# Kernel optimization log

Measured on AMD Instinct MI355X. Metric: run time of the kernel, lower is better.

The kernel has to match this reference:

```python
import jax, jax.numpy as jnp
import numpy as np

H = 256        # hidden_channels
G = 13         # num_input_geofeature
E = 100000     # number of 2nd-order triplets
N = 50000      # num_nodes
DEPTH = 3      # finaldepth
EPS = 1e-5     # BatchNorm eps


def setup_inputs() -> dict:
    key = jax.random.key(0)
    ks = jax.random.split(key, 10)
    d_in = 3 * H + G  # 781
    return {
        "node_feature": jax.random.normal(ks[0], (N, H), jnp.float32),
        "geo_encoding": jax.random.normal(ks[1], (E, G), jnp.float32),
        "edge_index_2rd": jax.random.randint(ks[2], (3, E), 0, N),
        "edx_ij": jax.random.randint(ks[3], (E,), 0, 2 * E),
        "edx_jk": jax.random.randint(ks[4], (E,), 0, 2 * E),
        "att": jax.random.uniform(ks[5], (4,), jnp.float32),
        # 4 branches: layer0 (d_in->H) + DEPTH layers (H->H), xavier-ish init, zero bias
        "W0": jax.random.normal(ks[6], (4, d_in, H), jnp.float32) * (1.0 / np.sqrt(d_in)),
        "b0": jnp.zeros((4, H), jnp.float32),
        "Wh": jax.random.normal(ks[7], (4, DEPTH, H, H), jnp.float32) * (1.0 / np.sqrt(H)),
        "bh": jnp.zeros((4, DEPTH, H), jnp.float32),
        # BatchNorm (eval mode): affine params + running stats, one per layer per branch
        "gamma": jnp.ones((4, DEPTH + 1, H), jnp.float32),
        "beta": jnp.zeros((4, DEPTH + 1, H), jnp.float32),
        "run_mean": jnp.zeros((4, DEPTH + 1, H), jnp.float32),
        "run_var": jnp.ones((4, DEPTH + 1, H), jnp.float32),
        "num_edge_inside": E,
        "num_nodes": N,
    }


def _bn(h, g, b, m, v):
    return (h - m) * jax.lax.rsqrt(v + EPS) * g + b


def reference(node_feature, geo_encoding, edge_index_2rd, edx_ij, edx_jk, att,
              W0, b0, Wh, bh, gamma, beta, run_mean, run_var,
              num_edge_inside, num_nodes):
    i, j, k = edge_index_2rd[0], edge_index_2rd[1], edge_index_2rd[2]
    # gather node triplets + geo features -> [E, 3H+G]
    x = jnp.concatenate(
        [node_feature[i], node_feature[j], node_feature[k], geo_encoding], axis=-1)

    m_ij = edx_ij < num_edge_inside
    m_jk = edx_jk < num_edge_inside
    # 4 mutually-exclusive, exhaustive routing masks: [4, E]
    masks = jnp.stack([m_ij & m_jk, m_ij & ~m_jk, ~m_ij & m_jk, ~m_ij & ~m_jk])

    x_output = jnp.zeros((x.shape[0], H), x.dtype)
    for br in range(4):  # fixed small branch count
        h = jax.nn.relu(_bn(x @ W0[br] + b0[br],
                            gamma[br, 0], beta[br, 0], run_mean[br, 0], run_var[br, 0]))
        for l in range(DEPTH):
            h = jax.nn.relu(_bn(h @ Wh[br, l] + bh[br, l],
                                gamma[br, l + 1], beta[br, l + 1],
                                run_mean[br, l + 1], run_var[br, l + 1]))
        h = jax.nn.leaky_relu(h) * att[br]
        x_output = x_output + jnp.where(masks[br][:, None], h, jnp.zeros((), h.dtype))
    # scatter_add over target node index i -> [num_nodes, H]
    return jax.ops.segment_sum(x_output, i, num_segments=num_nodes)
```

## Files before the change

kernel.cpp:

```cpp
#include <hip/hip_runtime.h>
#include <hip/hip_bf16.h>
#include <stdint.h>

#define HCH 256
#define GEO 13
#define DEPTH 3
#define EPSBN 1e-5f
#define MFMA __builtin_amdgcn_mfma_f32_16x16x32_bf16

typedef __attribute__((ext_vector_type(8))) short short8;
typedef __attribute__((ext_vector_type(4))) float floatx4;

__device__ __forceinline__ short f2bs(float f) {
    unsigned u = __float_as_uint(f);
    unsigned r = (u + 0x7fffu + ((u >> 16) & 1u)) >> 16;
    return (short)r;
}

__global__ void k_prep(const float* __restrict__ W0, const float* __restrict__ Wh,
                       const float* __restrict__ b0, const float* __restrict__ bh,
                       const float* __restrict__ gm, const float* __restrict__ bt,
                       const float* __restrict__ mn, const float* __restrict__ vr,
                       const float* __restrict__ att,
                       const float* __restrict__ node, const float* __restrict__ geo,
                       const int* __restrict__ edx_ij, const int* __restrict__ edx_jk,
                       const int* __restrict__ nei_p,
                       short* __restrict__ W0t, short* __restrict__ Wht,
                       float* __restrict__ sc, float* __restrict__ of,
                       short* __restrict__ node_bf, short* __restrict__ geo_bf,
                       int* __restrict__ lists, int* __restrict__ cnt,
                       float4* __restrict__ outz, int n4out,
                       int E, int d_in_dim, int nb_node, int nb_geo, int nb_out) {
    const int B_W0 = 100, B_WH = 96, B_SC = 16;
    __shared__ short s[32][256];
    int b = blockIdx.x, t = threadIdx.x;
    if (b < B_W0) {
        int c = b % 25, br = b / 25;
        #pragma unroll
        for (int kk = 0; kk < 32; ++kk) {
            int kidx = c * 32 + kk;
            float v = (kidx < d_in_dim) ? W0[((size_t)br * d_in_dim + kidx) * HCH + t] : 0.f;
            s[kk][t] = f2bs(v);
        }
        __syncthreads();
        size_t obase = ((size_t)(b) * 256 + t) * 32;
        #pragma unroll
        for (int g = 0; g < 4; ++g) {
            short8 v;
            #pragma unroll
            for (int j = 0; j < 8; ++j) v[j] = s[g * 8 + j][t];
            *reinterpret_cast<short8*>(W0t + obase + g * 8) = v;
        }
    } else if (b < B_W0 + B_WH) {
        int idx = b - B_W0;
        int c = idx & 7; idx >>= 3;
        int l = idx % 3, br = idx / 3;
        #pragma unroll
        for (int kk = 0; kk < 32; ++kk) {
            float v = Wh[((size_t)(br * DEPTH + l) * HCH + (c * 32 + kk)) * HCH + t];
            s[kk][t] = f2bs(v);
        }
        __syncthreads();
        size_t obase = ((size_t)(b - B_W0) * 256 + t) * 32;
        #pragma unroll
        for (int g = 0; g < 4; ++g) {
            short8 v;
            #pragma unroll
            for (int j = 0; j < 8; ++j) v[j] = s[g * 8 + j][t];
            *reinterpret_cast<short8*>(Wht + obase + g * 8) = v;
        }
    } else if (b < B_W0 + B_WH + B_SC) {
        int idx = (b - B_W0 - B_WH) * 256 + t;
        int col = idx & 255, l = (idx >> 8) & 3, br = idx >> 10;
        int gi = (br * (DEPTH + 1) + l) * HCH + col;
        float sA = gm[gi] * rsqrtf(vr[gi] + EPSBN);
        float bias = (l == 0) ? b0[br * HCH + col] : bh[(br * DEPTH + (l - 1)) * HCH + col];
        float ofv = (bias - mn[gi]) * sA + bt[gi];
        if (l == 3) { float av = att[br]; sA *= av; ofv *= av; }
        sc[idx] = sA;
        of[idx] = ofv;
    } else if (b < B_W0 + B_WH + B_SC + nb_node) {
        size_t i = ((size_t)(b - B_W0 - B_WH - B_SC) * 256 + t) * 8;
        const float4* src = reinterpret_cast<const float4*>(node + i);
        float4 v0 = src[0], v1 = src[1];
        short8 pk;
        pk[0] = f2bs(v0.x); pk[1] = f2bs(v0.y); pk[2] = f2bs(v0.z); pk[3] = f2bs(v0.w);
        pk[4] = f2bs(v1.x); pk[5] = f2bs(v1.y); pk[6] = f2bs(v1.z); pk[7] = f2bs(v1.w);
        *reinterpret_cast<short8*>(node_bf + i) = pk;
    } else if (b < B_W0 + B_WH + B_SC + nb_node + nb_geo) {
        int i = (b - B_W0 - B_WH - B_SC - nb_node) * 256 + t;
        int e = i >> 2, cc = i & 3;
        if (e < E) {
            short8 pk;
            #pragma unroll
            for (int j = 0; j < 8; ++j) {
                int col = cc * 8 + j;
                pk[j] = (col < GEO) ? f2bs(geo[(size_t)e * GEO + col]) : (short)0;
            }
            *reinterpret_cast<short8*>(geo_bf + (size_t)e * 32 + cc * 8) = pk;
        }
    } else if (b < B_W0 + B_WH + B_SC + nb_node + nb_geo + nb_out) {
        int i = (b - (B_W0 + B_WH + B_SC + nb_node + nb_geo)) * 256 + t;
        if (i < n4out) outz[i] = make_float4(0.f, 0.f, 0.f, 0.f);
    } else {
        int e = (b - (B_W0 + B_WH + B_SC + nb_node + nb_geo + nb_out)) * 256 + t;
        int NEI = nei_p[0];
        int lane = t & 63;
        int br = -1;
        if (e < E)
            br = ((edx_ij[e] < NEI) ? 0 : 2) + ((edx_jk[e] < NEI) ? 0 : 1);
        unsigned long long lt = (lane == 63) ? 0x7fffffffffffffffull
                                             : ((1ull << lane) - 1ull);
        #pragma unroll
        for (int bb = 0; bb < 4; ++bb) {
            unsigned long long mk = __ballot(br == bb);
            if (mk) {
                int leader = __ffsll((long long)mk) - 1;
                int base = 0;
                if (lane == leader) base = atomicAdd(&cnt[bb], (int)__popcll(mk));
                base = __shfl(base, leader);
                if (br == bb) {
                    int pos = base + (int)__popcll(mk & lt);
                    lists[(size_t)bb * E + pos] = e;
                }
            }
        }
    }
}

__global__ __launch_bounds__(512)
void k_main(const short* __restrict__ node_bf, const short* __restrict__ geo_bf,
            const int* __restrict__ eidx,
            const short* __restrict__ W0t, const short* __restrict__ Wht,
            const float* __restrict__ sc, const float* __restrict__ of,
            const int* __restrict__ lists, const int* __restrict__ cnt,
            float* __restrict__ out, int E) {
    __shared__ __align__(16) short A[64][264];
    __shared__ __align__(16) short Ageo[64][40];
    __shared__ int s_idx[3][64];
    __shared__ int s_e[64];

    int nwg = gridDim.x;
    int q = nwg >> 3, r = nwg & 7;
    int xcd = blockIdx.x & 7, jj = blockIdx.x >> 3;
    int b = ((xcd < r) ? xcd * (q + 1) : r * (q + 1) + (xcd - r) * q) + jj;

    int c0 = cnt[0], c1 = cnt[1], c2 = cnt[2], c3 = cnt[3];
    int t0 = (c0 + 63) >> 6, t1 = (c1 + 63) >> 6, t2 = (c2 + 63) >> 6, t3 = (c3 + 63) >> 6;
    int br, tile, count;
    if (b < t0)                     { br = 0; tile = b;                count = c0; }
    else if (b < t0 + t1)           { br = 1; tile = b - t0;           count = c1; }
    else if (b < t0 + t1 + t2)      { br = 2; tile = b - t0 - t1;      count = c2; }
    else if (b < t0 + t1 + t2 + t3) { br = 3; tile = b - t0 - t1 - t2; count = c3; }
    else return;
    int m = count - tile * 64; if (m > 64) m = 64;

    int t = threadIdx.x;
    if (t < 64) {
        int e = (t < m) ? lists[(size_t)br * E + (size_t)tile * 64 + t] : 0;
        s_e[t] = (t < m) ? e : -1;
        s_idx[0][t] = eidx[e];
        s_idx[1][t] = eidx[E + e];
        s_idx[2][t] = eidx[2 * E + e];
    }
    __syncthreads();

    int wv = t >> 6, lane = t & 63, quad = lane >> 4, l16 = lane & 15;
    int rbase = t >> 5, cc8 = (t & 31) * 8;

    floatx4 acc[4][2];
    #pragma unroll
    for (int rt = 0; rt < 4; ++rt)
        #pragma unroll
        for (int ct = 0; ct < 2; ++ct)
            #pragma unroll
            for (int r2 = 0; r2 < 4; ++r2) acc[rt][ct][r2] = 0.f;

    int boff[2];
    #pragma unroll
    for (int ct = 0; ct < 2; ++ct)
        boff[ct] = (wv * 32 + ct * 16 + l16) * 32 + quad * 8;

    short* Ag = &Ageo[0][0];

    auto do_chunks8 = [&](const short* Wbase) {
        short8 bb[3][2];
        #pragma unroll
        for (int ct = 0; ct < 2; ++ct) {
            bb[0][ct] = *reinterpret_cast<const short8*>(Wbase + boff[ct]);
            bb[1][ct] = *reinterpret_cast<const short8*>(Wbase + 8192 + boff[ct]);
        }
        #pragma unroll
        for (int c = 0; c < 8; ++c) {
            if (c + 2 < 8) {
                const short* Bn = Wbase + (size_t)(c + 2) * 8192;
                #pragma unroll
                for (int ct = 0; ct < 2; ++ct)
                    bb[(c + 2) % 3][ct] = *reinterpret_cast<const short8*>(Bn + boff[ct]);
            }
            short8 af[4];
            #pragma unroll
            for (int rt = 0; rt < 4; ++rt)
                af[rt] = *reinterpret_cast<const short8*>(&A[rt * 16 + l16][c * 32 + quad * 8]);
            #pragma unroll
            for (int rt = 0; rt < 4; ++rt)
                #pragma unroll
                for (int ct = 0; ct < 2; ++ct)
                    acc[rt][ct] = MFMA(af[rt], bb[c % 3][ct], acc[rt][ct], 0, 0, 0);
        }
    };
    auto do_chunk1 = [&](const short* Wbase) {
        short8 bc[2];
        #pragma unroll
        for (int ct = 0; ct < 2; ++ct)
            bc[ct] = *reinterpret_cast<const short8*>(Wbase + boff[ct]);
        short8 af[4];
        #pragma unroll
        for (int rt = 0; rt < 4; ++rt)
            af[rt] = *reinterpret_cast<const short8*>(Ag + (rt * 16 + l16) * 40 + quad * 8);
        #pragma unroll
        for (int rt = 0; rt < 4; ++rt)
            #pragma unroll
            for (int ct = 0; ct < 2; ++ct)
                acc[rt][ct] = MFMA(af[rt], bc[ct], acc[rt][ct], 0, 0, 0);
    };

    if (t < 256) {
        int grow = t >> 2, gp = (t & 3) * 8;
        int ge = s_e[grow];
        short8 gv;
        if (ge >= 0) gv = *reinterpret_cast<const short8*>(geo_bf + (size_t)ge * 32 + gp);
        else {
            #pragma unroll
            for (int j = 0; j < 8; ++j) gv[j] = 0;
        }
        *reinterpret_cast<short8*>(Ag + grow * 40 + gp) = gv;
    }
    short8 g[2][4];
    #pragma unroll
    for (int it = 0; it < 4; ++it)
        g[0][it] = *reinterpret_cast<const short8*>(
            node_bf + (size_t)s_idx[0][it * 16 + rbase] * HCH + cc8);

    #pragma unroll
    for (int p = 0; p < 3; ++p) {
        __syncthreads();
        #pragma unroll
        for (int it = 0; it < 4; ++it)
            *reinterpret_cast<short8*>(&A[it * 16 + rbase][cc8]) = g[p & 1][it];
        __syncthreads();
        if (p < 2) {
            const int* idxs = s_idx[p + 1];
            #pragma unroll
            for (int it = 0; it < 4; ++it)
                g[(p + 1) & 1][it] = *reinterpret_cast<const short8*>(
                    node_bf + (size_t)idxs[it * 16 + rbase] * HCH + cc8);
        }
        do_chunks8(W0t + (size_t)(br * 25 + p * 8) * 8192);
    }
    do_chunk1(W0t + (size_t)(br * 25 + 24) * 8192);

    for (int l = 0; l < 4; ++l) {
        float sv[2], ov[2];
        #pragma unroll
        for (int ct = 0; ct < 2; ++ct) {
            int col = wv * 32 + ct * 16 + l16;
            sv[ct] = sc[(br * 4 + l) * HCH + col];
            ov[ct] = of[(br * 4 + l) * HCH + col];
        }
        if (l < 3) {
            __syncthreads();
            #pragma unroll
            for (int rt = 0; rt < 4; ++rt)
                #pragma unroll
                for (int ct = 0; ct < 2; ++ct) {
                    int col = wv * 32 + ct * 16 + l16;
                    #pragma unroll
                    for (int r2 = 0; r2 < 4; ++r2) {
                        int row = rt * 16 + quad * 4 + r2;
                        float h = fmaxf(acc[rt][ct][r2] * sv[ct] + ov[ct], 0.f);
                        A[row][col] = f2bs(h);
                        acc[rt][ct][r2] = 0.f;
                    }
                }
            __syncthreads();
            do_chunks8(Wht + (size_t)((br * 3 + l) * 8) * 8192);
        } else {
            #pragma unroll
            for (int rt = 0; rt < 4; ++rt)
                #pragma unroll
                for (int r2 = 0; r2 < 4; ++r2) {
                    int row = rt * 16 + quad * 4 + r2;
                    if (row < m) {
                        float* orow = out + (size_t)s_idx[0][row] * HCH + wv * 32 + l16;
                        #pragma unroll
                        for (int ct = 0; ct < 2; ++ct) {
                            float h = fmaxf(acc[rt][ct][r2] * sv[ct] + ov[ct], 0.f);
                            atomicAdd(orow + ct * 16, h);
                        }
                    }
                }
        }
    }
}

extern "C" void kernel_launch(void* const* d_in, const int* in_sizes, int n_in,
                              void* d_out, int out_size, void* d_ws, size_t ws_size,
                              hipStream_t stream) {
    const float* node  = (const float*)d_in[0];
    const float* geo   = (const float*)d_in[1];
    const int*   eidx  = (const int*)d_in[2];
    const int*   edxij = (const int*)d_in[3];
    const int*   edxjk = (const int*)d_in[4];
    const float* att   = (const float*)d_in[5];
    const float* W0    = (const float*)d_in[6];
    const float* b0    = (const float*)d_in[7];
    const float* Wh    = (const float*)d_in[8];
    const float* bh    = (const float*)d_in[9];
    const float* gm    = (const float*)d_in[10];
    const float* bt    = (const float*)d_in[11];
    const float* mn    = (const float*)d_in[12];
    const float* vr    = (const float*)d_in[13];
    const int*   neip  = (const int*)d_in[14];

    int E = in_sizes[3];
    int N = in_sizes[0] / HCH;
    int d_in_dim = in_sizes[6] / (4 * HCH);

    uint8_t* w = (uint8_t*)d_ws;
    size_t off = 0;
    short* W0t  = (short*)(w + off); off += (size_t)4 * 25 * 256 * 32 * 2;
    short* Wht  = (short*)(w + off); off += (size_t)4 * 3 * 8 * 256 * 32 * 2;
    float* sc   = (float*)(w + off); off += 4096 * 4;
    float* of   = (float*)(w + off); off += 4096 * 4;
    int*   lists= (int*)(w + off);   off += (size_t)4 * E * 4;
    int*   cnt  = (int*)(w + off);   off += 16;
    short* node_bf = (short*)(w + off); off += (size_t)N * HCH * 2;
    short* geo_bf  = (short*)(w + off); off += (size_t)E * 32 * 2;

    float* out = (float*)d_out;
    int n4 = out_size / 4;

    hipMemsetAsync(cnt, 0, 16, stream);

    int nb_node = N / 8;
    int nb_geo  = (4 * E + 255) / 256;
    int nb_out  = (n4 + 255) / 256;
    int nb_cmp  = (E + 255) / 256;
    k_prep<<<100 + 96 + 16 + nb_node + nb_geo + nb_out + nb_cmp, 256, 0, stream>>>(
        W0, Wh, b0, bh, gm, bt, mn, vr, att, node, geo, edxij, edxjk, neip,
        W0t, Wht, sc, of, node_bf, geo_bf, lists, cnt,
        (float4*)out, n4, E, d_in_dim, nb_node, nb_geo, nb_out);

    int T = (E >> 6) + 8;
    k_main<<<T, 512, 0, stream>>>(node_bf, geo_bf, eidx, W0t, Wht,
                                  sc, of, lists, cnt, out, E);
}
```

Measured before the change: 393.7 us.

## Stage gathered node rows directly into LDS with XOR swizzle

Gathered node-feature rows now go straight from global memory into LDS through global_load_lds. This replaces the register double-buffered gather and the separate LDS stores. The padded LDS tile becomes an unpadded XOR-swizzled layout to avoid bank conflicts, and the reads and epilogue writes are updated to match. The XCD-aware block remapping is removed and the weight prefetch is moved after the MFMAs. The cost is that the gather of the next input slice no longer overlaps compute, since each stage now waits at barriers.

```diff
diff --git a/kernel.cpp b/kernel.cpp
--- a/kernel.cpp
+++ b/kernel.cpp
@@ -10,6 +10,9 @@
 
 typedef __attribute__((ext_vector_type(8))) short short8;
 typedef __attribute__((ext_vector_type(4))) float floatx4;
+
+typedef __attribute__((address_space(1))) const void g_void;
+typedef __attribute__((address_space(3))) void l_void;
 
 __device__ __forceinline__ short f2bs(float f) {
     unsigned u = __float_as_uint(f);
@@ -135,18 +138,14 @@
             const float* __restrict__ sc, const float* __restrict__ of,
             const int* __restrict__ lists, const int* __restrict__ cnt,
             float* __restrict__ out, int E) {
-    __shared__ __align__(16) short A[64][264];
+    __shared__ __align__(16) short A[64][256];
     __shared__ __align__(16) short Ageo[64][40];
     __shared__ int s_idx[3][64];
     __shared__ int s_e[64];
 
-    int nwg = gridDim.x;
-    int q = nwg >> 3, r = nwg & 7;
-    int xcd = blockIdx.x & 7, jj = blockIdx.x >> 3;
-    int b = ((xcd < r) ? xcd * (q + 1) : r * (q + 1) + (xcd - r) * q) + jj;
-
     int c0 = cnt[0], c1 = cnt[1], c2 = cnt[2], c3 = cnt[3];
     int t0 = (c0 + 63) >> 6, t1 = (c1 + 63) >> 6, t2 = (c2 + 63) >> 6, t3 = (c3 + 63) >> 6;
+    int b = blockIdx.x;
     int br, tile, count;
     if (b < t0)                     { br = 0; tile = b;                count = c0; }
     else if (b < t0 + t1)           { br = 1; tile = b - t0;           count = c1; }
@@ -165,8 +164,8 @@
     }
     __syncthreads();
 
-    int wv = t >> 6, lane = t & 63, quad = lane >> 4, l16 = lane & 15;
-    int rbase = t >> 5, cc8 = (t & 31) * 8;
+    int wvid = t >> 6, lane = t & 63, quad = lane >> 4, l16 = lane & 15;
+    int swz = (l16 & 7) << 4;
 
     floatx4 acc[4][2];
     #pragma unroll
@@ -179,9 +178,23 @@
     int boff[2];
     #pragma unroll
     for (int ct = 0; ct < 2; ++ct)
-        boff[ct] = (wv * 32 + ct * 16 + l16) * 32 + quad * 8;
-
+        boff[ct] = (wvid * 32 + ct * 16 + l16) * 32 + quad * 8;
+
+    const char* Ab = (const char*)&A[0][0];
+    char* Aw = (char*)&A[0][0];
     short* Ag = &Ageo[0][0];
+
+    auto stage_nodes = [&](const int* idxp) {
+        #pragma unroll
+        for (int i = 0; i < 4; ++i) {
+            int r0 = wvid * 8 + i * 2;
+            int row = r0 + (lane >> 5);
+            int e = idxp[row];
+            int soff = ((lane & 31) * 16) ^ ((row & 7) << 4);
+            const char* src = (const char*)(node_bf + (size_t)e * HCH) + soff;
+            __builtin_amdgcn_global_load_lds((g_void*)src, (l_void*)(&A[r0][0]), 16, 0, 0);
+        }
+    };
 
     auto do_chunks8 = [&](const short* Wbase) {
         short8 bb[3][2];
@@ -192,21 +205,22 @@
         }
         #pragma unroll
         for (int c = 0; c < 8; ++c) {
+            short8 af[4];
+            #pragma unroll
+            for (int rt = 0; rt < 4; ++rt)
+                af[rt] = *reinterpret_cast<const short8*>(
+                    Ab + (rt * 16 + l16) * 512 + ((c * 64 + quad * 16) ^ swz));
+            #pragma unroll
+            for (int rt = 0; rt < 4; ++rt)
+                #pragma unroll
+                for (int ct = 0; ct < 2; ++ct)
+                    acc[rt][ct] = MFMA(af[rt], bb[c % 3][ct], acc[rt][ct], 0, 0, 0);
             if (c + 2 < 8) {
                 const short* Bn = Wbase + (size_t)(c + 2) * 8192;
                 #pragma unroll
                 for (int ct = 0; ct < 2; ++ct)
                     bb[(c + 2) % 3][ct] = *reinterpret_cast<const short8*>(Bn + boff[ct]);
             }
-            short8 af[4];
-            #pragma unroll
-            for (int rt = 0; rt < 4; ++rt)
-                af[rt] = *reinterpret_cast<const short8*>(&A[rt * 16 + l16][c * 32 + quad * 8]);
-            #pragma unroll
-            for (int rt = 0; rt < 4; ++rt)
-                #pragma unroll
-                for (int ct = 0; ct < 2; ++ct)
-                    acc[rt][ct] = MFMA(af[rt], bb[c % 3][ct], acc[rt][ct], 0, 0, 0);
         }
     };
     auto do_chunk1 = [&](const short* Wbase) {
@@ -236,35 +250,27 @@
         }
         *reinterpret_cast<short8*>(Ag + grow * 40 + gp) = gv;
     }
-    short8 g[2][4];
-    #pragma unroll
-    for (int it = 0; it < 4; ++it)
-        g[0][it] = *reinterpret_cast<const short8*>(
-            node_bf + (size_t)s_idx[0][it * 16 + rbase] * HCH + cc8);
-
-    #pragma unroll
-    for (int p = 0; p < 3; ++p) {
-        __syncthreads();
-        #pragma unroll
-        for (int it = 0; it < 4; ++it)
-            *reinterpret_cast<short8*>(&A[it * 16 + rbase][cc8]) = g[p & 1][it];
-        __syncthreads();
-        if (p < 2) {
-            const int* idxs = s_idx[p + 1];
-            #pragma unroll
-            for (int it = 0; it < 4; ++it)
-                g[(p + 1) & 1][it] = *reinterpret_cast<const short8*>(
-                    node_bf + (size_t)idxs[it * 16 + rbase] * HCH + cc8);
-        }
-        do_chunks8(W0t + (size_t)(br * 25 + p * 8) * 8192);
-    }
+    stage_nodes(s_idx[0]);
+    __syncthreads();
+
+    do_chunks8(W0t + (size_t)(br * 25 + 0) * 8192);
+    __syncthreads();
+    stage_nodes(s_idx[1]);
+    __syncthreads();
+
+    do_chunks8(W0t + (size_t)(br * 25 + 8) * 8192);
+    __syncthreads();
+    stage_nodes(s_idx[2]);
+    __syncthreads();
+
+    do_chunks8(W0t + (size_t)(br * 25 + 16) * 8192);
     do_chunk1(W0t + (size_t)(br * 25 + 24) * 8192);
 
     for (int l = 0; l < 4; ++l) {
         float sv[2], ov[2];
         #pragma unroll
         for (int ct = 0; ct < 2; ++ct) {
-            int col = wv * 32 + ct * 16 + l16;
+            int col = wvid * 32 + ct * 16 + l16;
             sv[ct] = sc[(br * 4 + l) * HCH + col];
             ov[ct] = of[(br * 4 + l) * HCH + col];
         }
@@ -274,12 +280,13 @@
             for (int rt = 0; rt < 4; ++rt)
                 #pragma unroll
                 for (int ct = 0; ct < 2; ++ct) {
-                    int col = wv * 32 + ct * 16 + l16;
+                    int colb = (wvid * 32 + ct * 16 + l16) * 2;
                     #pragma unroll
                     for (int r2 = 0; r2 < 4; ++r2) {
                         int row = rt * 16 + quad * 4 + r2;
                         float h = fmaxf(acc[rt][ct][r2] * sv[ct] + ov[ct], 0.f);
-                        A[row][col] = f2bs(h);
+                        *reinterpret_cast<short*>(
+                            Aw + row * 512 + (colb ^ ((row & 7) << 4))) = f2bs(h);
                         acc[rt][ct][r2] = 0.f;
                     }
                 }
@@ -292,7 +299,7 @@
                 for (int r2 = 0; r2 < 4; ++r2) {
                     int row = rt * 16 + quad * 4 + r2;
                     if (row < m) {
-                        float* orow = out + (size_t)s_idx[0][row] * HCH + wv * 32 + l16;
+                        float* orow = out + (size_t)s_idx[0][row] * HCH + wvid * 32 + l16;
                         #pragma unroll
                         for (int ct = 0; ct < 2; ++ct) {
                             float h = fmaxf(acc[rt][ct][r2] * sv[ct] + ov[ct], 0.f);
```

Measured after the change: 427.4 us. 8.6% more time.
